# Kernel tuning notes

Hardware: AMD Instinct MI355X
Metric: run time of the kernel (lower is better)

Reference implementation:

```python
import jax, jax.numpy as jnp
import numpy as np

VOCAB = 256
BIG = 128
NN = 1024  # nodes per LSTM layer


def setup_inputs() -> dict:
    key = jax.random.key(0)
    ks = jax.random.split(key, 10)
    T, B = 512, 128
    in_dim = VOCAB + 2 + 1  # one-hot char + 2 speaker flags + bot flag
    emb = 512

    def w(k, shape, fan_in):
        return jax.random.normal(k, shape, dtype=jnp.float32) * np.float32(1.0 / np.sqrt(fan_in))

    return {
        "inputs": jax.random.normal(ks[0], (T, B, in_dim), dtype=jnp.float32),
        "emb_W": w(ks[1], (in_dim, emb), in_dim),
        "lstm_W0": w(ks[2], (emb + BIG + NN, 4 * NN), emb + BIG + NN),
        "lstm_b0": jnp.zeros((4 * NN,), dtype=jnp.float32),
        "lstm_W1": w(ks[3], (NN + NN, 4 * NN), NN + NN),
        "lstm_b1": jnp.zeros((4 * NN,), dtype=jnp.float32),
        "out_W0": w(ks[4], (NN, NN), NN),
        "out_b0": jnp.zeros((NN,), dtype=jnp.float32),
        "out_W1": w(ks[5], (NN, VOCAB), NN),
        "out_b1": jnp.zeros((VOCAB,), dtype=jnp.float32),
    }


def _lstm_cell(x, h, c, W, b, nn):
    # concat + matmul + bias, split [3nn | nn], sigmoid/tanh gating
    z = jnp.concatenate([x, h], axis=1) @ W + b  # [B, 4nn]
    sigm = jax.nn.sigmoid(z[:, : 3 * nn])
    trans = jnp.tanh(z[:, 3 * nn :])
    f, i, o = sigm[:, :nn], sigm[:, nn : 2 * nn], sigm[:, 2 * nn :]
    c_new = f * c + i * trans
    h_new = o * jnp.tanh(c_new)
    return h_new, c_new


def reference(inputs, emb_W, lstm_W0, lstm_b0, lstm_W1, lstm_b1,
              out_W0, out_b0, out_W1, out_b1):
    T, B, _ = inputs.shape
    first_speaker = jnp.array([[1.0, 0.0]], dtype=inputs.dtype)

    def step(carry, inp_t):
        h0, c0, h1, c1 = carry
        # embed (dropout keep_prob = 1.0)
        emb = inp_t @ emb_W  # [B, emb]
        # attach big flag: +/-1 tile depending on speaker flag == [1, 0]
        flag = inp_t[:, VOCAB : VOCAB + 2]
        comp = jnp.prod((flag == first_speaker).astype(inp_t.dtype), axis=1, keepdims=True)
        comp = jax.lax.stop_gradient(comp)
        big = jnp.tile((comp - 0.5) * 2.0, (1, BIG))  # [B, BIG]
        x = jnp.concatenate([emb, big], axis=1)
        # 2-layer LSTM stack
        h0, c0 = _lstm_cell(x, h0, c0, lstm_W0, lstm_b0, NN)
        h1, c1 = _lstm_cell(h0, h1, c1, lstm_W1, lstm_b1, NN)
        # output module: Linear -> ReLU -> Linear
        hs = jax.nn.relu(h1 @ out_W0 + out_b0)
        logits = hs @ out_W1 + out_b1  # [B, VOCAB]
        return (h0, c0, h1, c1), logits

    zeros = jnp.zeros((B, NN), dtype=inputs.dtype)
    init = (zeros, zeros, zeros, zeros)
    _, logits = jax.lax.scan(step, init, inputs)  # [T, B, VOCAB]
    return logits
```

## Files before the change

kernel.cpp:

```cpp
#include <hip/hip_runtime.h>
#include <hip/hip_bf16.h>
#include <math.h>

typedef unsigned short u16;
typedef short short8v __attribute__((ext_vector_type(8)));
typedef float f32x4 __attribute__((ext_vector_type(4)));

#define TT 512
#define BB 128
#define IND 259
#define KPWF 384

#define LDS_BYTES 30720

__device__ __forceinline__ u16 f2bf(float x) {
    __hip_bfloat16 h = __float2bfloat16(x);
    return *reinterpret_cast<u16*>(&h);
}
__device__ __forceinline__ float bf2f(u16 u) {
    unsigned v = ((unsigned)u) << 16;
    return __uint_as_float(v);
}
__device__ __forceinline__ void splitbf(float x, u16& hi, u16& lo) {
    hi = f2bf(x);
    lo = f2bf(x - bf2f(hi));
}

__global__ __launch_bounds__(256) void k_zero(float* __restrict__ p, int n) {
    int i = blockIdx.x * 256 + threadIdx.x;
    int stride = gridDim.x * 256;
    for (; i < n; i += stride) p[i] = 0.f;
}

__global__ __launch_bounds__(256) void k_fold(const float* __restrict__ embW,
                                              const float* __restrict__ W0,
                                              float* __restrict__ WF) {
    int j = blockIdx.x * 256 + threadIdx.x;
    int i = blockIdx.y;
    float acc = 0.f;
    for (int e = 0; e < 512; ++e)
        acc += embW[i * 512 + e] * W0[(size_t)e * 4096 + j];
    WF[(size_t)i * 4096 + j] = acc;
}

__global__ __launch_bounds__(256) void k_S(const float* __restrict__ W0, float* __restrict__ S) {
    int j = blockIdx.x * 256 + threadIdx.x;
    float acc = 0.f;
    for (int r = 0; r < 128; ++r)
        acc += W0[(size_t)(512 + r) * 4096 + j];
    S[j] = acc;
}

__global__ __launch_bounds__(256) void k_sgn(const float* __restrict__ inp, float* __restrict__ sgn) {
    int i = blockIdx.x * 256 + threadIdx.x;
    float f0 = inp[(size_t)i * IND + 256];
    float f1 = inp[(size_t)i * IND + 257];
    sgn[i] = (f0 == 1.0f && f1 == 0.0f) ? 1.0f : -1.0f;
}

__global__ __launch_bounds__(256) void k_split(const float* __restrict__ src, int srcStride,
                                               int K, int Kpad, int perm,
                                               u16* __restrict__ hi, u16* __restrict__ lo) {
    int col = blockIdx.y;
    int k = blockIdx.x * 256 + threadIdx.x;
    if (k >= Kpad) return;
    int j = col;
    if (perm) {
        int c = col & 15, g = (col >> 4) & 3, hs = col >> 6;
        j = g * 1024 + hs * 16 + c;
    }
    float v = (k < K) ? src[(size_t)k * srcStride + j] : 0.f;
    u16 h, l; splitbf(v, h, l);
    hi[(size_t)col * Kpad + k] = h;
    lo[(size_t)col * Kpad + k] = l;
}

template<int NC, int AMODE>
__device__ __forceinline__ void gemm_core(
    char* smem, int tid,
    const u16* Ah0, const u16* Al0,
    const u16* Ah1, const u16* Al1,
    int phsw,
    const float* Af,
    const u16* Bh, int ldb,
    int bmode, int bhalf,
    int nkt,
    f32x4 (&acc)[2][NC/32])
{
    constexpr int APL  = 64 * 80;
    constexpr int BPL  = NC * 80;
    constexpr int BUFB = 2 * APL + BPL;
    const int lane = tid & 63, wid = tid >> 6;
    const int wrg = wid >> 1, wcg = wid & 1;
    const int rlo = lane & 15, khi = lane >> 4;

    const int srow = tid >> 2;
    const int sk8  = (tid & 3) * 8;
    int bcol, bq;
    if (NC == 64) { bcol = tid >> 2; bq = tid & 3; }
    else          { bcol = tid >> 3; bq = tid & 7; }
    int bcg = bcol;
    if (bmode) bcg = ((bcol >> 3) * 16) + bhalf * 8 + (bcol & 7);

    uint4 ra0, ra1, rb4;
    uint2 rb2;
    float rf[8];

    auto LOADF = [&](int tile) {
        if constexpr (AMODE == 0) {
            const u16* pAh = Ah0; const u16* pAl = Al0; int kk = tile * 32;
            if (tile >= phsw) { pAh = Ah1; pAl = Al1; kk = (tile - phsw) * 32; }
            ra0 = *(const uint4*)(pAh + (size_t)srow * 1024 + kk + sk8);
            ra1 = *(const uint4*)(pAl + (size_t)srow * 1024 + kk + sk8);
        } else {
            const float* sa = Af + (size_t)srow * IND;
            int k0 = tile * 32 + sk8;
            #pragma unroll
            for (int j = 0; j < 8; ++j) rf[j] = (k0 + j < IND) ? sa[k0 + j] : 0.f;
        }
        if constexpr (NC == 64) {
            rb4 = *(const uint4*)(Bh + (size_t)bcg * ldb + tile * 32 + bq * 8);
        } else {
            rb2 = *(const uint2*)(Bh + (size_t)bcg * ldb + tile * 32 + bq * 4);
        }
    };
    auto WRITEF = [&](int tile) {
        char* buf = smem + (tile & 1) * BUFB;
        char* d = buf + srow * 80 + sk8 * 2;
        if constexpr (AMODE == 0) {
            *(uint4*)d = ra0;
            *(uint4*)(d + APL) = ra1;
        } else {
            alignas(16) u16 hb[8], lb[8];
            #pragma unroll
            for (int j = 0; j < 8; ++j) splitbf(rf[j], hb[j], lb[j]);
            *(uint4*)d = *(const uint4*)hb;
            *(uint4*)(d + APL) = *(const uint4*)lb;
        }
        char* e = buf + 2 * APL + bcol * 80;
        if constexpr (NC == 64) {
            *(uint4*)(e + bq * 16) = rb4;
        } else {
            *(uint2*)(e + bq * 8) = rb2;
        }
    };
    auto COMPUTEF = [&](int kt) {
        const char* buf = smem + (kt & 1) * BUFB;
        short8v ah[2], al[2], bh[NC/32];
        #pragma unroll
        for (int rfi = 0; rfi < 2; ++rfi) {
            int row = wrg * 32 + rfi * 16 + rlo;
            const char* p = buf + row * 80 + khi * 16;
            ah[rfi] = *(const short8v*)p;
            al[rfi] = *(const short8v*)(p + APL);
        }
        #pragma unroll
        for (int cfi = 0; cfi < NC/32; ++cfi) {
            int col = wcg * (NC/2) + cfi * 16 + rlo;
            bh[cfi] = *(const short8v*)(buf + 2 * APL + col * 80 + khi * 16);
        }
        #pragma unroll
        for (int rfi = 0; rfi < 2; ++rfi)
            #pragma unroll
            for (int cfi = 0; cfi < NC/32; ++cfi) {
                acc[rfi][cfi] = __builtin_amdgcn_mfma_f32_16x16x32_bf16(ah[rfi], bh[cfi], acc[rfi][cfi], 0, 0, 0);
                acc[rfi][cfi] = __builtin_amdgcn_mfma_f32_16x16x32_bf16(al[rfi], bh[cfi], acc[rfi][cfi], 0, 0, 0);
            }
    };

    LOADF(0); WRITEF(0); __syncthreads();
    for (int kt = 0; kt < nkt; ++kt) {
        if (kt + 1 < nkt) LOADF(kt + 1);
        COMPUTEF(kt);
        if (kt + 1 < nkt) WRITEF(kt + 1);
        __syncthreads();
    }
}

template<int NC>
__device__ __forceinline__ void store_zs(char* smem, int tid, f32x4 (&acc)[2][NC/32], int ncp) {
    float* zs = (float*)smem;
    const int lane = tid & 63, wid = tid >> 6;
    const int wrg = wid >> 1, wcg = wid & 1;
    const int rlo = lane & 15, khi = lane >> 4;
    #pragma unroll
    for (int rfi = 0; rfi < 2; ++rfi)
        #pragma unroll
        for (int cfi = 0; cfi < NC/32; ++cfi)
            #pragma unroll
            for (int r = 0; r < 4; ++r)
                zs[(wrg*32 + rfi*16 + khi*4 + r) * ncp + wcg*(NC/2) + cfi*16 + rlo] = acc[rfi][cfi][r];
}

struct SArgs {
    const float *inp, *Sv, *SG, *b0, *b1;
    const u16 *WFh, *W0h, *W1h;
    u16 *h0h0, *h0l0, *h0h1, *h0l1;
    u16 *ringh, *ringl;
    float *Zin, *c0, *c1;
    int R, t;
};

__global__ __launch_bounds__(256) void k_step(SArgs a) {
    extern __shared__ char smem[];
    const int bid = blockIdx.x, tid = threadIdx.x;
    const int t = a.t;

    if (bid < 128) {
        if (t < 0 || t >= TT) return;
        const int mb = bid >> 6, hs = bid & 63;
        const int m0 = mb * 64;
        f32x4 acc[2][2];
        #pragma unroll
        for (int i = 0; i < 2; ++i) { acc[i][0] = (f32x4)0.f; acc[i][1] = (f32x4)0.f; }
        const u16* Ah = (((t - 1) & 1) ? a.h0h1 : a.h0h0) + (size_t)m0 * 1024;
        const u16* Al = (((t - 1) & 1) ? a.h0l1 : a.h0l0) + (size_t)m0 * 1024;
        gemm_core<64,0>(smem, tid, Ah, Al, Ah, Al, 99, nullptr,
                        a.W0h + (size_t)hs*64*1024, 1024,
                        0, 0, 32, acc);
        store_zs<64>(smem, tid, acc, 68);
        __syncthreads();
        float* zs = (float*)smem;
        const float* zin = a.Zin + (size_t)(t & 1) * BB * 4096;
        u16* hoh = ((t & 1) ? a.h0h1 : a.h0h0);
        u16* hol = ((t & 1) ? a.h0l1 : a.h0l0);
        #pragma unroll
        for (int i = 0; i < 4; ++i) {
            int q = tid + 256 * i;
            int row = q >> 4, c16 = q & 15;
            int grow = m0 + row;
            int hid = hs * 16 + c16;
            float sg = a.SG[(size_t)t * BB + grow];
            const float* zr = zs + row * 68;
            const float* zn = zin + (size_t)grow * 4096 + hs * 64;
            float zF = zr[c16]      + zn[c16]      + sg * a.Sv[hid]        + a.b0[hid];
            float zI = zr[16 + c16] + zn[16 + c16] + sg * a.Sv[1024 + hid] + a.b0[1024 + hid];
            float zO = zr[32 + c16] + zn[32 + c16] + sg * a.Sv[2048 + hid] + a.b0[2048 + hid];
            float zG = zr[48 + c16] + zn[48 + c16] + sg * a.Sv[3072 + hid] + a.b0[3072 + hid];
            float f = 1.f / (1.f + expf(-zF));
            float ii = 1.f / (1.f + expf(-zI));
            float o = 1.f / (1.f + expf(-zO));
            float g = tanhf(zG);
            size_t ci = (size_t)grow * 1024 + hid;
            float cn = f * a.c0[ci] + ii * g;
            a.c0[ci] = cn;
            float h = o * tanhf(cn);
            u16 hh, hl; splitbf(h, hh, hl);
            hoh[ci] = hh; hol[ci] = hl;
        }
    } else if (bid < 384) {
        const int tau = t - 1;
        if (tau < 0 || tau >= TT) return;
        const int bb = bid - 128;
        const int mb = bb >> 7, sub = bb & 127;
        const int hs = sub >> 1, half = sub & 1;
        const int m0 = mb * 64;
        f32x4 acc[2][1];
        #pragma unroll
        for (int i = 0; i < 2; ++i) acc[i][0] = (f32x4)0.f;
        const u16* A0h = (((tau & 1) ? a.h0h1 : a.h0h0)) + (size_t)m0 * 1024;
        const u16* A0l = (((tau & 1) ? a.h0l1 : a.h0l0)) + (size_t)m0 * 1024;
        int slotr = (tau - 1 + a.R) % a.R;
        const u16* A1h = a.ringh + (size_t)slotr * BB * 1024 + (size_t)m0 * 1024;
        const u16* A1l = a.ringl + (size_t)slotr * BB * 1024 + (size_t)m0 * 1024;
        gemm_core<32,0>(smem, tid, A0h, A0l, A1h, A1l, 32, nullptr,
                        a.W1h + (size_t)hs*64*2048, 2048,
                        1, half, 64, acc);
        store_zs<32>(smem, tid, acc, 36);
        __syncthreads();
        float* zs = (float*)smem;
        int slotw = tau % a.R;
        u16* rh = a.ringh + (size_t)slotw * BB * 1024;
        u16* rl = a.ringl + (size_t)slotw * BB * 1024;
        #pragma unroll
        for (int i = 0; i < 2; ++i) {
            int q = tid + 256 * i;
            int row = q >> 3, c8 = q & 7;
            int grow = m0 + row;
            int hid = hs * 16 + half * 8 + c8;
            const float* zr = zs + row * 36;
            float zF = zr[c8]      + a.b1[hid];
            float zI = zr[8 + c8]  + a.b1[1024 + hid];
            float zO = zr[16 + c8] + a.b1[2048 + hid];
            float zG = zr[24 + c8] + a.b1[3072 + hid];
            float f = 1.f / (1.f + expf(-zF));
            float ii = 1.f / (1.f + expf(-zI));
            float o = 1.f / (1.f + expf(-zO));
            float g = tanhf(zG);
            size_t ci = (size_t)grow * 1024 + hid;
            float cn = f * a.c1[ci] + ii * g;
            a.c1[ci] = cn;
            float h = o * tanhf(cn);
            u16 hh, hl; splitbf(h, hh, hl);
            rh[ci] = hh; rl[ci] = hl;
        }
    } else {
        const int tz = t + 1;
        if (tz < 0 || tz >= TT) return;
        const int zb = bid - 384;
        const int mb = zb >> 6, cwg = zb & 63;
        const int m0 = mb * 64;
        const int col0 = cwg * 64;
        f32x4 acc[2][2];
        #pragma unroll
        for (int i = 0; i < 2; ++i) { acc[i][0] = (f32x4)0.f; acc[i][1] = (f32x4)0.f; }
        const float* Af = a.inp + (size_t)tz * BB * IND + (size_t)m0 * IND;
        gemm_core<64,1>(smem, tid, nullptr, nullptr, nullptr, nullptr, 999, Af,
                        a.WFh + (size_t)col0 * KPWF, KPWF,
                        0, 0, KPWF / 32, acc);
        float* zo = a.Zin + (size_t)(tz & 1) * BB * 4096;
        const int lane = tid & 63, wid = tid >> 6;
        const int wrg = wid >> 1, wcg = wid & 1;
        const int rlo = lane & 15, khi = lane >> 4;
        #pragma unroll
        for (int rfi = 0; rfi < 2; ++rfi)
            #pragma unroll
            for (int cfi = 0; cfi < 2; ++cfi)
                #pragma unroll
                for (int r = 0; r < 4; ++r)
                    zo[(size_t)(m0 + wrg*32 + rfi*16 + khi*4 + r) * 4096 + col0 + wcg*32 + cfi*16 + rlo] = acc[rfi][cfi][r];
    }
}

__global__ __launch_bounds__(256) void k_head1(const u16* __restrict__ ringh, const u16* __restrict__ ringl,
                                               const u16* __restrict__ Wh,
                                               const float* __restrict__ bias,
                                               u16* __restrict__ hsh, u16* __restrict__ hsl) {
    extern __shared__ char smem[];
    const int tid = threadIdx.x;
    const int nb = blockIdx.x, mb = blockIdx.y;
    const size_t m0 = (size_t)mb * 64;
    f32x4 acc[2][2];
    #pragma unroll
    for (int i = 0; i < 2; ++i) { acc[i][0] = (f32x4)0.f; acc[i][1] = (f32x4)0.f; }
    const u16* Ah = ringh + m0 * 1024;
    const u16* Al = ringl + m0 * 1024;
    gemm_core<64,0>(smem, tid, Ah, Al, Ah, Al, 99, nullptr,
                    Wh + (size_t)nb*64*1024, 1024,
                    0, 0, 32, acc);
    const int lane = tid & 63, wid = tid >> 6;
    const int wrg = wid >> 1, wcg = wid & 1;
    const int rlo = lane & 15, khi = lane >> 4;
    #pragma unroll
    for (int rfi = 0; rfi < 2; ++rfi)
        #pragma unroll
        for (int cfi = 0; cfi < 2; ++cfi)
            #pragma unroll
            for (int r = 0; r < 4; ++r) {
                int row = wrg*32 + rfi*16 + khi*4 + r;
                int col = nb*64 + wcg*32 + cfi*16 + rlo;
                float v = acc[rfi][cfi][r] + bias[col];
                v = fmaxf(v, 0.f);
                u16 hh, hl; splitbf(v, hh, hl);
                size_t o = (m0 + row) * 1024 + col;
                hsh[o] = hh; hsl[o] = hl;
            }
}

__global__ __launch_bounds__(256) void k_head2(const u16* __restrict__ hsh, const u16* __restrict__ hsl,
                                               const u16* __restrict__ Wh,
                                               const float* __restrict__ bias,
                                               float* __restrict__ outp) {
    extern __shared__ char smem[];
    const int tid = threadIdx.x;
    const int nb = blockIdx.x, mb = blockIdx.y;
    const size_t m0 = (size_t)mb * 64;
    f32x4 acc[2][2];
    #pragma unroll
    for (int i = 0; i < 2; ++i) { acc[i][0] = (f32x4)0.f; acc[i][1] = (f32x4)0.f; }
    const u16* Ah = hsh + m0 * 1024;
    const u16* Al = hsl + m0 * 1024;
    gemm_core<64,0>(smem, tid, Ah, Al, Ah, Al, 99, nullptr,
                    Wh + (size_t)nb*64*1024, 1024,
                    0, 0, 32, acc);
    const int lane = tid & 63, wid = tid >> 6;
    const int wrg = wid >> 1, wcg = wid & 1;
    const int rlo = lane & 15, khi = lane >> 4;
    #pragma unroll
    for (int rfi = 0; rfi < 2; ++rfi)
        #pragma unroll
        for (int cfi = 0; cfi < 2; ++cfi)
            #pragma unroll
            for (int r = 0; r < 4; ++r) {
                int row = wrg*32 + rfi*16 + khi*4 + r;
                int col = nb*64 + wcg*32 + cfi*16 + rlo;
                outp[(m0 + row) * 256 + col] = acc[rfi][cfi][r] + bias[col];
            }
}

extern "C" void kernel_launch(void* const* d_in, const int* in_sizes, int n_in,
                              void* d_out, int out_size, void* d_ws, size_t ws_size,
                              hipStream_t stream)
{
    (void)in_sizes; (void)n_in; (void)out_size;
    const float* inputs = (const float*)d_in[0];
    const float* embW   = (const float*)d_in[1];
    const float* W0     = (const float*)d_in[2];
    const float* b0     = (const float*)d_in[3];
    const float* W1     = (const float*)d_in[4];
    const float* b1     = (const float*)d_in[5];
    const float* oW0    = (const float*)d_in[6];
    const float* ob0    = (const float*)d_in[7];
    const float* oW1    = (const float*)d_in[8];
    const float* ob1    = (const float*)d_in[9];
    float* out = (float*)d_out;

    char* base = (char*)d_ws;
    size_t off = 0;
    auto take = [&](size_t n) -> char* {
        size_t a = (off + 255) & ~(size_t)255;
        char* r = base + a;
        off = a + n;
        return r;
    };

    u16* WFh = (u16*)take(4096ull * KPWF * 2);
    u16* WFl = (u16*)take(4096ull * KPWF * 2);
    u16* W0h = (u16*)take(4096ull * 1024 * 2);
    u16* W0l = (u16*)take(4096ull * 1024 * 2);
    u16* W1h = (u16*)take(4096ull * 2048 * 2);
    u16* W1l = (u16*)take(4096ull * 2048 * 2);
    u16* oWAh = (u16*)take(1024ull * 1024 * 2);
    u16* oWAl = (u16*)take(1024ull * 1024 * 2);
    u16* oWBh = (u16*)take(256ull * 1024 * 2);
    u16* oWBl = (u16*)take(256ull * 1024 * 2);
    float* WFfold = (float*)take(259ull * 4096 * 4);
    float* Sv = (float*)take(4096 * 4);
    float* SG = (float*)take((size_t)TT * BB * 4);
    float* Zin = (float*)take(2ull * BB * 4096 * 4);
    u16* h0h0 = (u16*)take((size_t)BB * 1024 * 2);
    u16* h0l0 = (u16*)take((size_t)BB * 1024 * 2);
    u16* h0h1 = (u16*)take((size_t)BB * 1024 * 2);
    u16* h0l1 = (u16*)take((size_t)BB * 1024 * 2);
    float* c0 = (float*)take((size_t)BB * 1024 * 4);
    float* c1 = (float*)take((size_t)BB * 1024 * 4);

    size_t avail = (ws_size > off + (1u << 20)) ? (ws_size - off - (1u << 20)) : 0;
    int R = 512;
    while (R > 2 && (size_t)R * (BB * 1024ull * 2 * 4) > avail) R >>= 1;
    u16* ringh = (u16*)take((size_t)R * BB * 1024 * 2);
    u16* ringl = (u16*)take((size_t)R * BB * 1024 * 2);
    u16* hsh   = (u16*)take((size_t)R * BB * 1024 * 2);
    u16* hsl   = (u16*)take((size_t)R * BB * 1024 * 2);

    k_fold<<<dim3(16, 259), 256, 0, stream>>>(embW, W0, WFfold);
    k_S<<<16, 256, 0, stream>>>(W0, Sv);
    k_sgn<<<256, 256, 0, stream>>>(inputs, SG);
    k_split<<<dim3(2, 4096), 256, 0, stream>>>(WFfold, 4096, 259, KPWF, 1, WFh, WFl);
    k_split<<<dim3(4, 4096), 256, 0, stream>>>(W0 + 640ull * 4096, 4096, 1024, 1024, 1, W0h, W0l);
    k_split<<<dim3(8, 4096), 256, 0, stream>>>(W1, 4096, 2048, 2048, 1, W1h, W1l);
    k_split<<<dim3(4, 1024), 256, 0, stream>>>(oW0, 1024, 1024, 1024, 0, oWAh, oWAl);
    k_split<<<dim3(4, 256), 256, 0, stream>>>(oW1, 256, 1024, 1024, 0, oWBh, oWBl);
    k_zero<<<64, 256, 0, stream>>>(c0, BB * 1024);
    k_zero<<<64, 256, 0, stream>>>(c1, BB * 1024);
    k_zero<<<32, 256, 0, stream>>>((float*)h0h1, BB * 1024 / 2);
    k_zero<<<32, 256, 0, stream>>>((float*)h0l1, BB * 1024 / 2);
    k_zero<<<32, 256, 0, stream>>>((float*)(ringh + (size_t)(R - 1) * BB * 1024), BB * 1024 / 2);
    k_zero<<<32, 256, 0, stream>>>((float*)(ringl + (size_t)(R - 1) * BB * 1024), BB * 1024 / 2);

    SArgs a;
    a.inp = inputs; a.Sv = Sv; a.SG = SG; a.b0 = b0; a.b1 = b1;
    a.WFh = WFh; a.W0h = W0h; a.W1h = W1h;
    a.h0h0 = h0h0; a.h0l0 = h0l0; a.h0h1 = h0h1; a.h0l1 = h0l1;
    a.ringh = ringh; a.ringl = ringl;
    a.Zin = Zin; a.c0 = c0; a.c1 = c1;
    a.R = R;

    for (int L = -1; L <= TT; ++L) {
        a.t = L;
        k_step<<<512, 256, LDS_BYTES, stream>>>(a);
        if (L >= 1 && (L % R) == 0) {
            int c = L / R - 1;
            k_head1<<<dim3(16, R * 2), 256, LDS_BYTES, stream>>>(ringh, ringl, oWAh, ob0, hsh, hsl);
            k_head2<<<dim3(4, R * 2), 256, LDS_BYTES, stream>>>(hsh, hsl, oWBh, ob1,
                                                                out + (size_t)c * R * BB * 256);
        }
    }
}
```

Baseline: 15.28 ms.

## Load recurrent GEMM operands directly into MFMA registers and merge layer-1 column halves

The layer-0 and layer-1 recurrent GEMMs inside the per-step kernel now read A and B fragments straight from global memory into registers for MFMA, skipping the LDS staging and its barriers. Layer-1 blocks now each cover a full 64-column gate slice instead of two 32-column halves, so the layer-1 block count drops from 256 to 128 and the step grid from 512 to 384. The goal is lower per-step latency in this launch-bound recurrence. The cost is uncoalesced, L2-dependent global loads with no double buffering, plus fewer blocks to spread layer-1 work across CUs.

```diff
diff --git a/kernel.cpp b/kernel.cpp
--- a/kernel.cpp
+++ b/kernel.cpp
@@ -11,7 +11,8 @@
 #define IND 259
 #define KPWF 384
 
-#define LDS_BYTES 30720
+#define LDS_STEP 30720
+#define LDS_HEAD 30720
 
 __device__ __forceinline__ u16 f2bf(float x) {
     __hip_bfloat16 h = __float2bfloat16(x);
@@ -75,6 +76,45 @@
     lo[(size_t)col * Kpad + k] = l;
 }
 
+template<int NC>
+__device__ __forceinline__ void gemm_direct_seg(
+    int tid,
+    const u16* __restrict__ Ah, const u16* __restrict__ Al,
+    const u16* __restrict__ Bh, int ldb, int kb,
+    int cnt,
+    f32x4 (&acc)[2][NC/32])
+{
+    const int lane = tid & 63, wid = tid >> 6;
+    const int wrg = wid >> 1, wcg = wid & 1;
+    const int rlo = lane & 15, khi = lane >> 4;
+
+    const u16* a0 = Ah + (size_t)(wrg * 32 + rlo) * 1024 + khi * 8;
+    const u16* a1 = Ah + (size_t)(wrg * 32 + 16 + rlo) * 1024 + khi * 8;
+    const u16* l0 = Al + (size_t)(wrg * 32 + rlo) * 1024 + khi * 8;
+    const u16* l1 = Al + (size_t)(wrg * 32 + 16 + rlo) * 1024 + khi * 8;
+    const u16* b0 = Bh + (size_t)(wcg * (NC / 2) + rlo) * ldb + kb + khi * 8;
+    const u16* b1 = Bh + (size_t)(wcg * (NC / 2) + 16 + rlo) * ldb + kb + khi * 8;
+
+    #pragma unroll 4
+    for (int kt = 0; kt < cnt; ++kt) {
+        const int ko = kt * 32;
+        short8v vah[2], val2[2], vbh[NC / 32];
+        vah[0]  = *(const short8v*)(a0 + ko);
+        vah[1]  = *(const short8v*)(a1 + ko);
+        val2[0] = *(const short8v*)(l0 + ko);
+        val2[1] = *(const short8v*)(l1 + ko);
+        vbh[0]  = *(const short8v*)(b0 + ko);
+        if constexpr (NC == 64) vbh[1] = *(const short8v*)(b1 + ko);
+        #pragma unroll
+        for (int rfi = 0; rfi < 2; ++rfi)
+            #pragma unroll
+            for (int cfi = 0; cfi < NC / 32; ++cfi) {
+                acc[rfi][cfi] = __builtin_amdgcn_mfma_f32_16x16x32_bf16(vah[rfi],  vbh[cfi], acc[rfi][cfi], 0, 0, 0);
+                acc[rfi][cfi] = __builtin_amdgcn_mfma_f32_16x16x32_bf16(val2[rfi], vbh[cfi], acc[rfi][cfi], 0, 0, 0);
+            }
+    }
+}
+
 template<int NC, int AMODE>
 __device__ __forceinline__ void gemm_core(
     char* smem, int tid,
@@ -83,7 +123,6 @@
     int phsw,
     const float* Af,
     const u16* Bh, int ldb,
-    int bmode, int bhalf,
     int nkt,
     f32x4 (&acc)[2][NC/32])
 {
@@ -99,8 +138,6 @@
     int bcol, bq;
     if (NC == 64) { bcol = tid >> 2; bq = tid & 3; }
     else          { bcol = tid >> 3; bq = tid & 7; }
-    int bcg = bcol;
-    if (bmode) bcg = ((bcol >> 3) * 16) + bhalf * 8 + (bcol & 7);
 
     uint4 ra0, ra1, rb4;
     uint2 rb2;
@@ -119,9 +156,9 @@
             for (int j = 0; j < 8; ++j) rf[j] = (k0 + j < IND) ? sa[k0 + j] : 0.f;
         }
         if constexpr (NC == 64) {
-            rb4 = *(const uint4*)(Bh + (size_t)bcg * ldb + tile * 32 + bq * 8);
+            rb4 = *(const uint4*)(Bh + (size_t)bcol * ldb + tile * 32 + bq * 8);
         } else {
-            rb2 = *(const uint2*)(Bh + (size_t)bcg * ldb + tile * 32 + bq * 4);
+            rb2 = *(const uint2*)(Bh + (size_t)bcol * ldb + tile * 32 + bq * 4);
         }
     };
     auto WRITEF = [&](int tile) {
@@ -215,9 +252,7 @@
         for (int i = 0; i < 2; ++i) { acc[i][0] = (f32x4)0.f; acc[i][1] = (f32x4)0.f; }
         const u16* Ah = (((t - 1) & 1) ? a.h0h1 : a.h0h0) + (size_t)m0 * 1024;
         const u16* Al = (((t - 1) & 1) ? a.h0l1 : a.h0l0) + (size_t)m0 * 1024;
-        gemm_core<64,0>(smem, tid, Ah, Al, Ah, Al, 99, nullptr,
-                        a.W0h + (size_t)hs*64*1024, 1024,
-                        0, 0, 32, acc);
+        gemm_direct_seg<64>(tid, Ah, Al, a.W0h + (size_t)hs*64*1024, 1024, 0, 32, acc);
         store_zs<64>(smem, tid, acc, 68);
         __syncthreads();
         float* zs = (float*)smem;
@@ -248,41 +283,40 @@
             u16 hh, hl; splitbf(h, hh, hl);
             hoh[ci] = hh; hol[ci] = hl;
         }
-    } else if (bid < 384) {
+    } else if (bid < 256) {
         const int tau = t - 1;
         if (tau < 0 || tau >= TT) return;
         const int bb = bid - 128;
-        const int mb = bb >> 7, sub = bb & 127;
-        const int hs = sub >> 1, half = sub & 1;
+        const int mb = bb >> 6, hs = bb & 63;
         const int m0 = mb * 64;
-        f32x4 acc[2][1];
-        #pragma unroll
-        for (int i = 0; i < 2; ++i) acc[i][0] = (f32x4)0.f;
+        f32x4 acc[2][2];
+        #pragma unroll
+        for (int i = 0; i < 2; ++i) { acc[i][0] = (f32x4)0.f; acc[i][1] = (f32x4)0.f; }
         const u16* A0h = (((tau & 1) ? a.h0h1 : a.h0h0)) + (size_t)m0 * 1024;
         const u16* A0l = (((tau & 1) ? a.h0l1 : a.h0l0)) + (size_t)m0 * 1024;
         int slotr = (tau - 1 + a.R) % a.R;
         const u16* A1h = a.ringh + (size_t)slotr * BB * 1024 + (size_t)m0 * 1024;
         const u16* A1l = a.ringl + (size_t)slotr * BB * 1024 + (size_t)m0 * 1024;
-        gemm_core<32,0>(smem, tid, A0h, A0l, A1h, A1l, 32, nullptr,
-                        a.W1h + (size_t)hs*64*2048, 2048,
-                        1, half, 64, acc);
-        store_zs<32>(smem, tid, acc, 36);
+        const u16* Bh = a.W1h + (size_t)hs*64*2048;
+        gemm_direct_seg<64>(tid, A0h, A0l, Bh, 2048, 0,    32, acc);
+        gemm_direct_seg<64>(tid, A1h, A1l, Bh, 2048, 1024, 32, acc);
+        store_zs<64>(smem, tid, acc, 68);
         __syncthreads();
         float* zs = (float*)smem;
         int slotw = tau % a.R;
         u16* rh = a.ringh + (size_t)slotw * BB * 1024;
         u16* rl = a.ringl + (size_t)slotw * BB * 1024;
         #pragma unroll
-        for (int i = 0; i < 2; ++i) {
+        for (int i = 0; i < 4; ++i) {
             int q = tid + 256 * i;
-            int row = q >> 3, c8 = q & 7;
+            int row = q >> 4, c16 = q & 15;
             int grow = m0 + row;
-            int hid = hs * 16 + half * 8 + c8;
-            const float* zr = zs + row * 36;
-            float zF = zr[c8]      + a.b1[hid];
-            float zI = zr[8 + c8]  + a.b1[1024 + hid];
-            float zO = zr[16 + c8] + a.b1[2048 + hid];
-            float zG = zr[24 + c8] + a.b1[3072 + hid];
+            int hid = hs * 16 + c16;
+            const float* zr = zs + row * 68;
+            float zF = zr[c16]      + a.b1[hid];
+            float zI = zr[16 + c16] + a.b1[1024 + hid];
+            float zO = zr[32 + c16] + a.b1[2048 + hid];
+            float zG = zr[48 + c16] + a.b1[3072 + hid];
             float f = 1.f / (1.f + expf(-zF));
             float ii = 1.f / (1.f + expf(-zI));
             float o = 1.f / (1.f + expf(-zO));
@@ -297,7 +331,7 @@
     } else {
         const int tz = t + 1;
         if (tz < 0 || tz >= TT) return;
-        const int zb = bid - 384;
+        const int zb = bid - 256;
         const int mb = zb >> 6, cwg = zb & 63;
         const int m0 = mb * 64;
         const int col0 = cwg * 64;
@@ -307,7 +341,7 @@
         const float* Af = a.inp + (size_t)tz * BB * IND + (size_t)m0 * IND;
         gemm_core<64,1>(smem, tid, nullptr, nullptr, nullptr, nullptr, 999, Af,
                         a.WFh + (size_t)col0 * KPWF, KPWF,
-                        0, 0, KPWF / 32, acc);
+                        KPWF / 32, acc);
         float* zo = a.Zin + (size_t)(tz & 1) * BB * 4096;
         const int lane = tid & 63, wid = tid >> 6;
         const int wrg = wid >> 1, wcg = wid & 1;
@@ -337,7 +371,7 @@
     const u16* Al = ringl + m0 * 1024;
     gemm_core<64,0>(smem, tid, Ah, Al, Ah, Al, 99, nullptr,
                     Wh + (size_t)nb*64*1024, 1024,
-                    0, 0, 32, acc);
+                    32, acc);
     const int lane = tid & 63, wid = tid >> 6;
     const int wrg = wid >> 1, wcg = wid & 1;
     const int rlo = lane & 15, khi = lane >> 4;
@@ -372,7 +406,7 @@
     const u16* Al = hsl + m0 * 1024;
     gemm_core<64,0>(smem, tid, Ah, Al, Ah, Al, 99, nullptr,
                     Wh + (size_t)nb*64*1024, 1024,
-                    0, 0, 32, acc);
+                    32, acc);
     const int lane = tid & 63, wid = tid >> 6;
     const int wrg = wid >> 1, wcg = wid & 1;
     const int rlo = lane & 15, khi = lane >> 4;
@@ -468,12 +502,12 @@
 
     for (int L = -1; L <= TT; ++L) {
         a.t = L;
-        k_step<<<512, 256, LDS_BYTES, stream>>>(a);
+        k_step<<<384, 256, LDS_STEP, stream>>>(a);
         if (L >= 1 && (L % R) == 0) {
             int c = L / R - 1;
-            k_head1<<<dim3(16, R * 2), 256, LDS_BYTES, stream>>>(ringh, ringl, oWAh, ob0, hsh, hsl);
-            k_head2<<<dim3(4, R * 2), 256, LDS_BYTES, stream>>>(hsh, hsl, oWBh, ob1,
-                                                                out + (size_t)c * R * BB * 256);
+            k_head1<<<dim3(16, R * 2), 256, LDS_HEAD, stream>>>(ringh, ringl, oWAh, ob0, hsh, hsl);
+            k_head2<<<dim3(4, R * 2), 256, LDS_HEAD, stream>>>(hsh, hsl, oWBh, ob1,
+                                                               out + (size_t)c * R * BB * 256);
         }
     }
 }
```

Result: slower. 29.33 ms (+92.0%).

## Replace per-timestep kernel launches with a persistent cooperative kernel using grid sync

Applied to the files above, without the earlier changes.

Moves the roughly 514 per-step launches, plus the periodic head launches, into a single persistent cooperative kernel of 512 blocks. Each iteration ends with grid.sync(), and the output head GEMMs run as strided tasks inside the same kernel. The aim is to remove launch overhead and inter-kernel gaps between the many small steps. It requires all 512 blocks to be co-resident, and falls back to the old launch loop if the cooperative launch fails.

```diff
diff --git a/kernel.cpp b/kernel.cpp
--- a/kernel.cpp
+++ b/kernel.cpp
@@ -1,6 +1,9 @@
 #include <hip/hip_runtime.h>
 #include <hip/hip_bf16.h>
+#include <hip/hip_cooperative_groups.h>
 #include <math.h>
+
+namespace cg = cooperative_groups;
 
 typedef unsigned short u16;
 typedef short short8v __attribute__((ext_vector_type(8)));
@@ -192,200 +195,231 @@
                 zs[(wrg*32 + rfi*16 + khi*4 + r) * ncp + wcg*(NC/2) + cfi*16 + rlo] = acc[rfi][cfi][r];
 }
 
-struct SArgs {
-    const float *inp, *Sv, *SG, *b0, *b1;
-    const u16 *WFh, *W0h, *W1h;
+struct KArgs {
+    const float *inp, *Sv, *SG, *b0, *b1, *ob0, *ob1;
+    const u16 *WFh, *W0h, *W1h, *oWAh, *oWBh;
     u16 *h0h0, *h0l0, *h0h1, *h0l1;
-    u16 *ringh, *ringl;
+    u16 *ringh, *ringl, *hsh, *hsl;
     float *Zin, *c0, *c1;
+    float *out;
     int R, t;
 };
 
-__global__ __launch_bounds__(256) void k_step(SArgs a) {
+__device__ void cell0_work(char* smem, int tid, int bid, int t, const KArgs& a) {
+    const int mb = bid >> 6, hs = bid & 63;
+    const int m0 = mb * 64;
+    f32x4 acc[2][2];
+    #pragma unroll
+    for (int i = 0; i < 2; ++i) { acc[i][0] = (f32x4)0.f; acc[i][1] = (f32x4)0.f; }
+    const u16* Ah = (((t - 1) & 1) ? a.h0h1 : a.h0h0) + (size_t)m0 * 1024;
+    const u16* Al = (((t - 1) & 1) ? a.h0l1 : a.h0l0) + (size_t)m0 * 1024;
+    gemm_core<64,0>(smem, tid, Ah, Al, Ah, Al, 99, nullptr,
+                    a.W0h + (size_t)hs*64*1024, 1024, 0, 0, 32, acc);
+    store_zs<64>(smem, tid, acc, 68);
+    __syncthreads();
+    float* zs = (float*)smem;
+    const float* zin = a.Zin + (size_t)(t & 1) * BB * 4096;
+    u16* hoh = ((t & 1) ? a.h0h1 : a.h0h0);
+    u16* hol = ((t & 1) ? a.h0l1 : a.h0l0);
+    #pragma unroll
+    for (int i = 0; i < 4; ++i) {
+        int q = tid + 256 * i;
+        int row = q >> 4, c16 = q & 15;
+        int grow = m0 + row;
+        int hid = hs * 16 + c16;
+        float sg = a.SG[(size_t)t * BB + grow];
+        const float* zr = zs + row * 68;
+        const float* zn = zin + (size_t)grow * 4096 + hs * 64;
+        float zF = zr[c16]      + zn[c16]      + sg * a.Sv[hid]        + a.b0[hid];
+        float zI = zr[16 + c16] + zn[16 + c16] + sg * a.Sv[1024 + hid] + a.b0[1024 + hid];
+        float zO = zr[32 + c16] + zn[32 + c16] + sg * a.Sv[2048 + hid] + a.b0[2048 + hid];
+        float zG = zr[48 + c16] + zn[48 + c16] + sg * a.Sv[3072 + hid] + a.b0[3072 + hid];
+        float f = 1.f / (1.f + expf(-zF));
+        float ii = 1.f / (1.f + expf(-zI));
+        float o = 1.f / (1.f + expf(-zO));
+        float g = tanhf(zG);
+        size_t ci = (size_t)grow * 1024 + hid;
+        float cn = f * a.c0[ci] + ii * g;
+        a.c0[ci] = cn;
+        float h = o * tanhf(cn);
+        u16 hh, hl; splitbf(h, hh, hl);
+        hoh[ci] = hh; hol[ci] = hl;
+    }
+    __syncthreads();
+}
+
+__device__ void cell1_work(char* smem, int tid, int bb, int tau, const KArgs& a) {
+    const int mb = bb >> 7, sub = bb & 127;
+    const int hs = sub >> 1, half = sub & 1;
+    const int m0 = mb * 64;
+    f32x4 acc[2][1];
+    #pragma unroll
+    for (int i = 0; i < 2; ++i) acc[i][0] = (f32x4)0.f;
+    const u16* A0h = (((tau & 1) ? a.h0h1 : a.h0h0)) + (size_t)m0 * 1024;
+    const u16* A0l = (((tau & 1) ? a.h0l1 : a.h0l0)) + (size_t)m0 * 1024;
+    int slotr = (tau - 1 + a.R) % a.R;
+    const u16* A1h = a.ringh + (size_t)slotr * BB * 1024 + (size_t)m0 * 1024;
+    const u16* A1l = a.ringl + (size_t)slotr * BB * 1024 + (size_t)m0 * 1024;
+    gemm_core<32,0>(smem, tid, A0h, A0l, A1h, A1l, 32, nullptr,
+                    a.W1h + (size_t)hs*64*2048, 2048, 1, half, 64, acc);
+    store_zs<32>(smem, tid, acc, 36);
+    __syncthreads();
+    float* zs = (float*)smem;
+    int slotw = tau % a.R;
+    u16* rh = a.ringh + (size_t)slotw * BB * 1024;
+    u16* rl = a.ringl + (size_t)slotw * BB * 1024;
+    #pragma unroll
+    for (int i = 0; i < 2; ++i) {
+        int q = tid + 256 * i;
+        int row = q >> 3, c8 = q & 7;
+        int grow = m0 + row;
+        int hid = hs * 16 + half * 8 + c8;
+        const float* zr = zs + row * 36;
+        float zF = zr[c8]      + a.b1[hid];
+        float zI = zr[8 + c8]  + a.b1[1024 + hid];
+        float zO = zr[16 + c8] + a.b1[2048 + hid];
+        float zG = zr[24 + c8] + a.b1[3072 + hid];
+        float f = 1.f / (1.f + expf(-zF));
+        float ii = 1.f / (1.f + expf(-zI));
+        float o = 1.f / (1.f + expf(-zO));
+        float g = tanhf(zG);
+        size_t ci = (size_t)grow * 1024 + hid;
+        float cn = f * a.c1[ci] + ii * g;
+        a.c1[ci] = cn;
+        float h = o * tanhf(cn);
+        u16 hh, hl; splitbf(h, hh, hl);
+        rh[ci] = hh; rl[ci] = hl;
+    }
+    __syncthreads();
+}
+
+__device__ void zin_work(char* smem, int tid, int zb, int tz, const KArgs& a) {
+    const int mb = zb >> 6, cwg = zb & 63;
+    const int m0 = mb * 64;
+    const int col0 = cwg * 64;
+    f32x4 acc[2][2];
+    #pragma unroll
+    for (int i = 0; i < 2; ++i) { acc[i][0] = (f32x4)0.f; acc[i][1] = (f32x4)0.f; }
+    const float* Af = a.inp + (size_t)tz * BB * IND + (size_t)m0 * IND;
+    gemm_core<64,1>(smem, tid, nullptr, nullptr, nullptr, nullptr, 999, Af,
+                    a.WFh + (size_t)col0 * KPWF, KPWF, 0, 0, KPWF / 32, acc);
+    float* zo = a.Zin + (size_t)(tz & 1) * BB * 4096;
+    const int lane = tid & 63, wid = tid >> 6;
+    const int wrg = wid >> 1, wcg = wid & 1;
+    const int rlo = lane & 15, khi = lane >> 4;
+    #pragma unroll
+    for (int rfi = 0; rfi < 2; ++rfi)
+        #pragma unroll
+        for (int cfi = 0; cfi < 2; ++cfi)
+            #pragma unroll
+            for (int r = 0; r < 4; ++r)
+                zo[(size_t)(m0 + wrg*32 + rfi*16 + khi*4 + r) * 4096 + col0 + wcg*32 + cfi*16 + rlo] = acc[rfi][cfi][r];
+    __syncthreads();
+}
+
+__device__ void head1_work(char* smem, int tid, int mb, int nb, const KArgs& a) {
+    const size_t m0 = (size_t)mb * 64;
+    f32x4 acc[2][2];
+    #pragma unroll
+    for (int i = 0; i < 2; ++i) { acc[i][0] = (f32x4)0.f; acc[i][1] = (f32x4)0.f; }
+    const u16* Ah = a.ringh + m0 * 1024;
+    const u16* Al = a.ringl + m0 * 1024;
+    gemm_core<64,0>(smem, tid, Ah, Al, Ah, Al, 99, nullptr,
+                    a.oWAh + (size_t)nb*64*1024, 1024, 0, 0, 32, acc);
+    const int lane = tid & 63, wid = tid >> 6;
+    const int wrg = wid >> 1, wcg = wid & 1;
+    const int rlo = lane & 15, khi = lane >> 4;
+    #pragma unroll
+    for (int rfi = 0; rfi < 2; ++rfi)
+        #pragma unroll
+        for (int cfi = 0; cfi < 2; ++cfi)
+            #pragma unroll
+            for (int r = 0; r < 4; ++r) {
+                int row = wrg*32 + rfi*16 + khi*4 + r;
+                int col = nb*64 + wcg*32 + cfi*16 + rlo;
+                float v = acc[rfi][cfi][r] + a.ob0[col];
+                v = fmaxf(v, 0.f);
+                u16 hh, hl; splitbf(v, hh, hl);
+                size_t o = (m0 + row) * 1024 + col;
+                a.hsh[o] = hh; a.hsl[o] = hl;
+            }
+    __syncthreads();
+}
+
+__device__ void head2_work(char* smem, int tid, int mb, int nb, const KArgs& a, float* outp) {
+    const size_t m0 = (size_t)mb * 64;
+    f32x4 acc[2][2];
+    #pragma unroll
+    for (int i = 0; i < 2; ++i) { acc[i][0] = (f32x4)0.f; acc[i][1] = (f32x4)0.f; }
+    const u16* Ah = a.hsh + m0 * 1024;
+    const u16* Al = a.hsl + m0 * 1024;
+    gemm_core<64,0>(smem, tid, Ah, Al, Ah, Al, 99, nullptr,
+                    a.oWBh + (size_t)nb*64*1024, 1024, 0, 0, 32, acc);
+    const int lane = tid & 63, wid = tid >> 6;
+    const int wrg = wid >> 1, wcg = wid & 1;
+    const int rlo = lane & 15, khi = lane >> 4;
+    #pragma unroll
+    for (int rfi = 0; rfi < 2; ++rfi)
+        #pragma unroll
+        for (int cfi = 0; cfi < 2; ++cfi)
+            #pragma unroll
+            for (int r = 0; r < 4; ++r) {
+                int row = wrg*32 + rfi*16 + khi*4 + r;
+                int col = nb*64 + wcg*32 + cfi*16 + rlo;
+                outp[(m0 + row) * 256 + col] = acc[rfi][cfi][r] + a.ob1[col];
+            }
+    __syncthreads();
+}
+
+__global__ __launch_bounds__(256) void k_step(KArgs a) {
     extern __shared__ char smem[];
     const int bid = blockIdx.x, tid = threadIdx.x;
     const int t = a.t;
-
     if (bid < 128) {
-        if (t < 0 || t >= TT) return;
-        const int mb = bid >> 6, hs = bid & 63;
-        const int m0 = mb * 64;
-        f32x4 acc[2][2];
-        #pragma unroll
-        for (int i = 0; i < 2; ++i) { acc[i][0] = (f32x4)0.f; acc[i][1] = (f32x4)0.f; }
-        const u16* Ah = (((t - 1) & 1) ? a.h0h1 : a.h0h0) + (size_t)m0 * 1024;
-        const u16* Al = (((t - 1) & 1) ? a.h0l1 : a.h0l0) + (size_t)m0 * 1024;
-        gemm_core<64,0>(smem, tid, Ah, Al, Ah, Al, 99, nullptr,
-                        a.W0h + (size_t)hs*64*1024, 1024,
-                        0, 0, 32, acc);
-        store_zs<64>(smem, tid, acc, 68);
-        __syncthreads();
-        float* zs = (float*)smem;
-        const float* zin = a.Zin + (size_t)(t & 1) * BB * 4096;
-        u16* hoh = ((t & 1) ? a.h0h1 : a.h0h0);
-        u16* hol = ((t & 1) ? a.h0l1 : a.h0l0);
-        #pragma unroll
-        for (int i = 0; i < 4; ++i) {
-            int q = tid + 256 * i;
-            int row = q >> 4, c16 = q & 15;
-            int grow = m0 + row;
-            int hid = hs * 16 + c16;
-            float sg = a.SG[(size_t)t * BB + grow];
-            const float* zr = zs + row * 68;
-            const float* zn = zin + (size_t)grow * 4096 + hs * 64;
-            float zF = zr[c16]      + zn[c16]      + sg * a.Sv[hid]        + a.b0[hid];
-            float zI = zr[16 + c16] + zn[16 + c16] + sg * a.Sv[1024 + hid] + a.b0[1024 + hid];
-            float zO = zr[32 + c16] + zn[32 + c16] + sg * a.Sv[2048 + hid] + a.b0[2048 + hid];
-            float zG = zr[48 + c16] + zn[48 + c16] + sg * a.Sv[3072 + hid] + a.b0[3072 + hid];
-            float f = 1.f / (1.f + expf(-zF));
-            float ii = 1.f / (1.f + expf(-zI));
-            float o = 1.f / (1.f + expf(-zO));
-            float g = tanhf(zG);
-            size_t ci = (size_t)grow * 1024 + hid;
-            float cn = f * a.c0[ci] + ii * g;
-            a.c0[ci] = cn;
-            float h = o * tanhf(cn);
-            u16 hh, hl; splitbf(h, hh, hl);
-            hoh[ci] = hh; hol[ci] = hl;
-        }
+        if (t >= 0 && t < TT) cell0_work(smem, tid, bid, t, a);
     } else if (bid < 384) {
-        const int tau = t - 1;
-        if (tau < 0 || tau >= TT) return;
-        const int bb = bid - 128;
-        const int mb = bb >> 7, sub = bb & 127;
-        const int hs = sub >> 1, half = sub & 1;
-        const int m0 = mb * 64;
-        f32x4 acc[2][1];
-        #pragma unroll
-        for (int i = 0; i < 2; ++i) acc[i][0] = (f32x4)0.f;
-        const u16* A0h = (((tau & 1) ? a.h0h1 : a.h0h0)) + (size_t)m0 * 1024;
-        const u16* A0l = (((tau & 1) ? a.h0l1 : a.h0l0)) + (size_t)m0 * 1024;
-        int slotr = (tau - 1 + a.R) % a.R;
-        const u16* A1h = a.ringh + (size_t)slotr * BB * 1024 + (size_t)m0 * 1024;
-        const u16* A1l = a.ringl + (size_t)slotr * BB * 1024 + (size_t)m0 * 1024;
-        gemm_core<32,0>(smem, tid, A0h, A0l, A1h, A1l, 32, nullptr,
-                        a.W1h + (size_t)hs*64*2048, 2048,
-                        1, half, 64, acc);
-        store_zs<32>(smem, tid, acc, 36);
-        __syncthreads();
-        float* zs = (float*)smem;
-        int slotw = tau % a.R;
-        u16* rh = a.ringh + (size_t)slotw * BB * 1024;
-        u16* rl = a.ringl + (size_t)slotw * BB * 1024;
-        #pragma unroll
-        for (int i = 0; i < 2; ++i) {
-            int q = tid + 256 * i;
-            int row = q >> 3, c8 = q & 7;
-            int grow = m0 + row;
-            int hid = hs * 16 + half * 8 + c8;
-            const float* zr = zs + row * 36;
-            float zF = zr[c8]      + a.b1[hid];
-            float zI = zr[8 + c8]  + a.b1[1024 + hid];
-            float zO = zr[16 + c8] + a.b1[2048 + hid];
-            float zG = zr[24 + c8] + a.b1[3072 + hid];
-            float f = 1.f / (1.f + expf(-zF));
-            float ii = 1.f / (1.f + expf(-zI));
-            float o = 1.f / (1.f + expf(-zO));
-            float g = tanhf(zG);
-            size_t ci = (size_t)grow * 1024 + hid;
-            float cn = f * a.c1[ci] + ii * g;
-            a.c1[ci] = cn;
-            float h = o * tanhf(cn);
-            u16 hh, hl; splitbf(h, hh, hl);
-            rh[ci] = hh; rl[ci] = hl;
-        }
+        if (t - 1 >= 0 && t - 1 < TT) cell1_work(smem, tid, bid - 128, t - 1, a);
     } else {
-        const int tz = t + 1;
-        if (tz < 0 || tz >= TT) return;
-        const int zb = bid - 384;
-        const int mb = zb >> 6, cwg = zb & 63;
-        const int m0 = mb * 64;
-        const int col0 = cwg * 64;
-        f32x4 acc[2][2];
-        #pragma unroll
-        for (int i = 0; i < 2; ++i) { acc[i][0] = (f32x4)0.f; acc[i][1] = (f32x4)0.f; }
-        const float* Af = a.inp + (size_t)tz * BB * IND + (size_t)m0 * IND;
-        gemm_core<64,1>(smem, tid, nullptr, nullptr, nullptr, nullptr, 999, Af,
-                        a.WFh + (size_t)col0 * KPWF, KPWF,
-                        0, 0, KPWF / 32, acc);
-        float* zo = a.Zin + (size_t)(tz & 1) * BB * 4096;
-        const int lane = tid & 63, wid = tid >> 6;
-        const int wrg = wid >> 1, wcg = wid & 1;
-        const int rlo = lane & 15, khi = lane >> 4;
-        #pragma unroll
-        for (int rfi = 0; rfi < 2; ++rfi)
-            #pragma unroll
-            for (int cfi = 0; cfi < 2; ++cfi)
-                #pragma unroll
-                for (int r = 0; r < 4; ++r)
-                    zo[(size_t)(m0 + wrg*32 + rfi*16 + khi*4 + r) * 4096 + col0 + wcg*32 + cfi*16 + rlo] = acc[rfi][cfi][r];
-    }
-}
-
-__global__ __launch_bounds__(256) void k_head1(const u16* __restrict__ ringh, const u16* __restrict__ ringl,
-                                               const u16* __restrict__ Wh,
-                                               const float* __restrict__ bias,
-                                               u16* __restrict__ hsh, u16* __restrict__ hsl) {
+        if (t + 1 >= 0 && t + 1 < TT) zin_work(smem, tid, bid - 384, t + 1, a);
+    }
+}
+__global__ __launch_bounds__(256) void k_fH1(KArgs a) {
     extern __shared__ char smem[];
-    const int tid = threadIdx.x;
-    const int nb = blockIdx.x, mb = blockIdx.y;
-    const size_t m0 = (size_t)mb * 64;
-    f32x4 acc[2][2];
-    #pragma unroll
-    for (int i = 0; i < 2; ++i) { acc[i][0] = (f32x4)0.f; acc[i][1] = (f32x4)0.f; }
-    const u16* Ah = ringh + m0 * 1024;
-    const u16* Al = ringl + m0 * 1024;
-    gemm_core<64,0>(smem, tid, Ah, Al, Ah, Al, 99, nullptr,
-                    Wh + (size_t)nb*64*1024, 1024,
-                    0, 0, 32, acc);
-    const int lane = tid & 63, wid = tid >> 6;
-    const int wrg = wid >> 1, wcg = wid & 1;
-    const int rlo = lane & 15, khi = lane >> 4;
-    #pragma unroll
-    for (int rfi = 0; rfi < 2; ++rfi)
-        #pragma unroll
-        for (int cfi = 0; cfi < 2; ++cfi)
-            #pragma unroll
-            for (int r = 0; r < 4; ++r) {
-                int row = wrg*32 + rfi*16 + khi*4 + r;
-                int col = nb*64 + wcg*32 + cfi*16 + rlo;
-                float v = acc[rfi][cfi][r] + bias[col];
-                v = fmaxf(v, 0.f);
-                u16 hh, hl; splitbf(v, hh, hl);
-                size_t o = (m0 + row) * 1024 + col;
-                hsh[o] = hh; hsl[o] = hl;
-            }
-}
-
-__global__ __launch_bounds__(256) void k_head2(const u16* __restrict__ hsh, const u16* __restrict__ hsl,
-                                               const u16* __restrict__ Wh,
-                                               const float* __restrict__ bias,
-                                               float* __restrict__ outp) {
+    head1_work(smem, threadIdx.x, blockIdx.y, blockIdx.x, a);
+}
+__global__ __launch_bounds__(256) void k_fH2(KArgs a, float* outp) {
     extern __shared__ char smem[];
-    const int tid = threadIdx.x;
-    const int nb = blockIdx.x, mb = blockIdx.y;
-    const size_t m0 = (size_t)mb * 64;
-    f32x4 acc[2][2];
-    #pragma unroll
-    for (int i = 0; i < 2; ++i) { acc[i][0] = (f32x4)0.f; acc[i][1] = (f32x4)0.f; }
-    const u16* Ah = hsh + m0 * 1024;
-    const u16* Al = hsl + m0 * 1024;
-    gemm_core<64,0>(smem, tid, Ah, Al, Ah, Al, 99, nullptr,
-                    Wh + (size_t)nb*64*1024, 1024,
-                    0, 0, 32, acc);
-    const int lane = tid & 63, wid = tid >> 6;
-    const int wrg = wid >> 1, wcg = wid & 1;
-    const int rlo = lane & 15, khi = lane >> 4;
-    #pragma unroll
-    for (int rfi = 0; rfi < 2; ++rfi)
-        #pragma unroll
-        for (int cfi = 0; cfi < 2; ++cfi)
-            #pragma unroll
-            for (int r = 0; r < 4; ++r) {
-                int row = wrg*32 + rfi*16 + khi*4 + r;
-                int col = nb*64 + wcg*32 + cfi*16 + rlo;
-                outp[(m0 + row) * 256 + col] = acc[rfi][cfi][r] + bias[col];
-            }
+    head2_work(smem, threadIdx.x, blockIdx.y, blockIdx.x, a, outp);
+}
+
+__global__ __launch_bounds__(256) void k_persist(KArgs a) {
+    extern __shared__ char smem[];
+    cg::grid_group grid = cg::this_grid();
+    const int bid = blockIdx.x, tid = threadIdx.x;
+
+    for (int L = -1; L <= TT; ++L) {
+        if (bid < 128) {
+            if (L >= 0 && L < TT) cell0_work(smem, tid, bid, L, a);
+        } else if (bid < 384) {
+            if (L - 1 >= 0 && L - 1 < TT) cell1_work(smem, tid, bid - 128, L - 1, a);
+        } else {
+            if (L + 1 >= 0 && L + 1 < TT) zin_work(smem, tid, bid - 384, L + 1, a);
+        }
+        grid.sync();
+
+        if (L >= a.R && (L % a.R) == 0) {
+            int c = L / a.R - 1;
+            int nt1 = a.R * 2 * 16;
+            for (int task = bid; task < nt1; task += 512)
+                head1_work(smem, tid, task >> 4, task & 15, a);
+            grid.sync();
+            int nt2 = a.R * 2 * 4;
+            float* ob = a.out + (size_t)c * a.R * BB * 256;
+            for (int task = bid; task < nt2; task += 512)
+                head2_work(smem, tid, task >> 2, task & 3, a, ob);
+            grid.sync();
+        }
+    }
 }
 
 extern "C" void kernel_launch(void* const* d_in, const int* in_sizes, int n_in,
@@ -458,22 +492,27 @@
     k_zero<<<32, 256, 0, stream>>>((float*)(ringh + (size_t)(R - 1) * BB * 1024), BB * 1024 / 2);
     k_zero<<<32, 256, 0, stream>>>((float*)(ringl + (size_t)(R - 1) * BB * 1024), BB * 1024 / 2);
 
-    SArgs a;
-    a.inp = inputs; a.Sv = Sv; a.SG = SG; a.b0 = b0; a.b1 = b1;
-    a.WFh = WFh; a.W0h = W0h; a.W1h = W1h;
+    KArgs a;
+    a.inp = inputs; a.Sv = Sv; a.SG = SG; a.b0 = b0; a.b1 = b1; a.ob0 = ob0; a.ob1 = ob1;
+    a.WFh = WFh; a.W0h = W0h; a.W1h = W1h; a.oWAh = oWAh; a.oWBh = oWBh;
     a.h0h0 = h0h0; a.h0l0 = h0l0; a.h0h1 = h0h1; a.h0l1 = h0l1;
-    a.ringh = ringh; a.ringl = ringl;
-    a.Zin = Zin; a.c0 = c0; a.c1 = c1;
-    a.R = R;
-
-    for (int L = -1; L <= TT; ++L) {
-        a.t = L;
-        k_step<<<512, 256, LDS_BYTES, stream>>>(a);
-        if (L >= 1 && (L % R) == 0) {
-            int c = L / R - 1;
-            k_head1<<<dim3(16, R * 2), 256, LDS_BYTES, stream>>>(ringh, ringl, oWAh, ob0, hsh, hsl);
-            k_head2<<<dim3(4, R * 2), 256, LDS_BYTES, stream>>>(hsh, hsl, oWBh, ob1,
-                                                                out + (size_t)c * R * BB * 256);
-        }
-    }
-}
+    a.ringh = ringh; a.ringl = ringl; a.hsh = hsh; a.hsl = hsl;
+    a.Zin = Zin; a.c0 = c0; a.c1 = c1; a.out = out;
+    a.R = R; a.t = 0;
+
+    void* params[] = { &a };
+    hipError_t err = hipLaunchCooperativeKernel((void*)k_persist, dim3(512), dim3(256),
+                                                params, LDS_BYTES, stream);
+    if (err != hipSuccess) {
+        (void)hipGetLastError();
+        for (int L = -1; L <= TT; ++L) {
+            a.t = L;
+            k_step<<<512, 256, LDS_BYTES, stream>>>(a);
+            if (L >= 1 && (L % R) == 0) {
+                int c = L / R - 1;
+                k_fH1<<<dim3(16, R * 2), 256, LDS_BYTES, stream>>>(a);
+                k_fH2<<<dim3(4, R * 2), 256, LDS_BYTES, stream>>>(a, out + (size_t)c * R * BB * 256);
+            }
+        }
+    }
+}
```

Result: slower. 49.91 ms (+226.7%).
